# Performance work log

Measured on AMD Instinct MI355X. Metric: run time of the kernel, lower is better.

## Reference

```python
import jax, jax.numpy as jnp
import numpy as np

B, S, D, H = 2, 2048, 1024, 16
HD = D // H  # head_dim = 64


def setup_inputs() -> dict:
    key = jax.random.key(0)
    ks = jax.random.split(key, 6)
    scale = 0.02
    x = jax.random.normal(ks[0], (B, S, D), dtype=jnp.float32)
    Wq = jax.random.normal(ks[1], (D, D), dtype=jnp.float32) * scale
    Wk = jax.random.normal(ks[2], (D, D), dtype=jnp.float32) * scale
    Wv = jax.random.normal(ks[3], (D, D), dtype=jnp.float32) * scale
    Wo = jax.random.normal(ks[4], (D, D), dtype=jnp.float32) * scale
    bo = jnp.zeros((D,), dtype=jnp.float32)
    return {"x": x, "Wq": Wq, "Wk": Wk, "Wv": Wv, "Wo": Wo, "bo": bo}


def reference(x, Wq, Wk, Wv, Wo, bo):
    b, s, _ = x.shape
    # Linear projections (qkv_bias=False), split into heads: [b, h, s, hd]
    def split_heads(t):
        return t.reshape(b, s, H, HD).transpose(0, 2, 1, 3)
    q = split_heads(x @ Wq)
    k = split_heads(x @ Wk)
    v = split_heads(x @ Wv)
    # Scaled dot-product scores: [b, h, s, s]
    scores = jnp.einsum('bhqd,bhkd->bhqk', q, k) / jnp.sqrt(jnp.float32(HD))
    # Causal mask: triu(ones, diagonal=1) positions -> -inf
    causal = jnp.triu(jnp.ones((s, s), dtype=bool), k=1)
    scores = jnp.where(causal, -jnp.inf, scores)
    attn = jax.nn.softmax(scores, axis=-1)
    # dropout p=0.0 (eval-equivalent): identity
    ctx = jnp.einsum('bhqk,bhkd->bhqd', attn, v)  # [b, h, s, hd]
    ctx = ctx.transpose(0, 2, 1, 3).reshape(b, s, D)
    return ctx @ Wo + bo
```

## Files before the change

kernel.cpp:

```cpp
#include <hip/hip_runtime.h>
#include <math.h>

#define BB 2
#define SS 2048
#define DD 1024
#define HH 16
#define HD 64
#define MM (BB * SS)

typedef __bf16 bf16;
typedef __attribute__((ext_vector_type(8))) __bf16 bf16x8;
typedef __attribute__((ext_vector_type(4))) __bf16 bf16x4;
typedef __attribute__((ext_vector_type(4))) short short4v;
typedef __attribute__((ext_vector_type(4))) float f32x4;

#if __has_builtin(__builtin_amdgcn_exp2f)
#define EXP2F(x) __builtin_amdgcn_exp2f(x)
#else
#define EXP2F(x) exp2f(x)
#endif

__device__ __forceinline__ f32x4 pv_mfma16(bf16x4 a, short4v b, f32x4 c) {
    return __builtin_amdgcn_mfma_f32_16x16x16bf16_1k(
        __builtin_bit_cast(short4v, a), b, c, 0, 0, 0);
}

__device__ __forceinline__ void gld_lds16(const void* g, void* l) {
    __builtin_amdgcn_global_load_lds(
        (const __attribute__((address_space(1))) void*)g,
        (__attribute__((address_space(3))) void*)l, 16, 0, 0);
}

__global__ __launch_bounds__(256) void prep(
    const float* __restrict__ x,
    const float* __restrict__ W0, const float* __restrict__ W1,
    const float* __restrict__ W2, const float* __restrict__ W3,
    bf16* __restrict__ xb, bf16* __restrict__ Wt)
{
    __shared__ float tile[32][33];
    const int z = blockIdx.z;
    if (z < 4) {
        const float* W = (z == 0) ? W0 : (z == 1) ? W1 : (z == 2) ? W2 : W3;
        bf16* O = Wt + (size_t)z * DD * DD;
        const int tx = threadIdx.x & 31, ty = threadIdx.x >> 5;
        const int k0 = blockIdx.y * 32, n0 = blockIdx.x * 32;
#pragma unroll
        for (int i = 0; i < 4; ++i)
            tile[ty + i * 8][tx] = W[(size_t)(k0 + ty + i * 8) * DD + n0 + tx];
        __syncthreads();
#pragma unroll
        for (int i = 0; i < 4; ++i)
            O[(size_t)(n0 + ty + i * 8) * DD + k0 + tx] = (bf16)tile[tx][ty + i * 8];
    } else {
        const int lb = (z - 4) * 1024 + blockIdx.y * 32 + blockIdx.x;
        const size_t i = ((size_t)lb * 256 + threadIdx.x) * 8;
        const float4 a = *(const float4*)(x + i);
        const float4 b = *(const float4*)(x + i + 4);
        bf16x8 o;
        o[0] = (bf16)a.x; o[1] = (bf16)a.y; o[2] = (bf16)a.z; o[3] = (bf16)a.w;
        o[4] = (bf16)b.x; o[5] = (bf16)b.y; o[6] = (bf16)b.z; o[7] = (bf16)b.w;
        *(bf16x8*)(xb + i) = o;
    }
}

__device__ __forceinline__ void mfma_core(
    const bf16* __restrict__ A, const bf16* __restrict__ Bt,
    int bm, int bn, int K, bf16* As, bf16* Bs, f32x4 (&acc)[4][4])
{
    const int t = threadIdx.x;
    const int w = t >> 6;
    const int l16 = t & 15, quad = (t >> 4) & 3;
    const int wr = w >> 1, wc = w & 1;
    const int arow = t >> 2;
    const int achk = (((t & 3) ^ ((t >> 3) & 3)) << 3);

    const bf16* gA = A + (size_t)(bm + arow) * K + achk;
    const bf16* gB = Bt + (size_t)(bn + arow) * K + achk;
    bf16* lA = As + w * 512;
    bf16* lB = Bs + w * 512;

    const int swz = (l16 >> 1) & 3;
    int offA[4], offB[4];
#pragma unroll
    for (int i = 0; i < 4; ++i) {
        offA[i] = (wr * 64 + i * 16 + l16) * 32 + ((quad ^ swz) << 3);
        offB[i] = (wc * 64 + i * 16 + l16) * 32 + ((quad ^ swz) << 3);
    }

#define GSTAGE(BUF, KO) do {                                                  \
        gld_lds16(gA + (KO),                  lA + (BUF) * 4096);             \
        gld_lds16(gA + (size_t)64 * K + (KO), lA + (BUF) * 4096 + 2048);      \
        gld_lds16(gB + (KO),                  lB + (BUF) * 4096);             \
        gld_lds16(gB + (size_t)64 * K + (KO), lB + (BUF) * 4096 + 2048);      \
    } while (0)

#define GCOMPUTE(BUF) do {                                                    \
        const bf16* Ab = As + (BUF) * 4096;                                   \
        const bf16* Bb = Bs + (BUF) * 4096;                                   \
        bf16x8 af[4], bv[4];                                                  \
        _Pragma("unroll")                                                     \
        for (int i = 0; i < 4; ++i) {                                         \
            af[i] = *(const bf16x8*)(Ab + offA[i]);                           \
            bv[i] = *(const bf16x8*)(Bb + offB[i]);                           \
        }                                                                     \
        _Pragma("unroll")                                                     \
        for (int mi = 0; mi < 4; ++mi)                                        \
            _Pragma("unroll")                                                 \
            for (int ni = 0; ni < 4; ++ni)                                    \
                acc[mi][ni] = __builtin_amdgcn_mfma_f32_16x16x32_bf16(        \
                    af[mi], bv[ni], acc[mi][ni], 0, 0, 0);                    \
    } while (0)

#define GBAR() do {                                                           \
        asm volatile("s_barrier" ::: "memory");                               \
        __builtin_amdgcn_sched_barrier(0);                                    \
    } while (0)

    GSTAGE(0, 0);
    const int nk = K >> 5;
    for (int kt = 0; kt < nk; kt += 2) {
        GSTAGE(1, (kt + 1) << 5);
        asm volatile("s_waitcnt vmcnt(4)" ::: "memory");
        GBAR();
        GCOMPUTE(0);
        asm volatile("s_waitcnt lgkmcnt(0)" ::: "memory");
        GBAR();
        if (kt + 2 < nk) {
            GSTAGE(0, (kt + 2) << 5);
            asm volatile("s_waitcnt vmcnt(4)" ::: "memory");
        } else {
            asm volatile("s_waitcnt vmcnt(0)" ::: "memory");
        }
        GBAR();
        GCOMPUTE(1);
        asm volatile("s_waitcnt lgkmcnt(0)" ::: "memory");
        GBAR();
    }
#undef GBAR
#undef GCOMPUTE
#undef GSTAGE
}

__global__ __launch_bounds__(256) void gemm_qkv(
    const bf16* __restrict__ xb, const bf16* __restrict__ Wt,
    bf16* __restrict__ Qb, bf16* __restrict__ Kb, bf16* __restrict__ Vb)
{
    __shared__ __align__(16) bf16 As[2 * 128 * 32];
    __shared__ __align__(16) bf16 Bs[2 * 128 * 32];
    const int bm = blockIdx.y * 128, bn = blockIdx.x * 128, z = blockIdx.z;

    f32x4 acc[4][4] = {};
    mfma_core(xb, Wt + (size_t)z * DD * DD, bm, bn, DD, As, Bs, acc);

    const int t = threadIdx.x;
    const int w = t >> 6, l16 = t & 15, quad = (t >> 4) & 3;
    const int wr = w >> 1, wc = w & 1;
    bf16* outp = (z == 0) ? Qb : (z == 1) ? Kb : Vb;
    const float scl = (z == 0) ? 0.18033688011f : 1.0f;

#pragma unroll
    for (int mi = 0; mi < 4; ++mi) {
#pragma unroll
        for (int ni = 0; ni < 4; ++ni) {
            const int col = bn + wc * 64 + ni * 16 + l16;
            const int h = col >> 6, hd = col & 63;
#pragma unroll
            for (int r = 0; r < 4; ++r) {
                const int row = bm + wr * 64 + mi * 16 + quad * 4 + r;
                const int b = row >> 11, s = row & (SS - 1);
                size_t addr;
                if (z < 2) addr = ((size_t)((b * HH + h) * SS + s)) * HD + hd;
                else       addr = ((size_t)((b * HH + h) * HD + hd)) * SS + s;
                outp[addr] = (bf16)(acc[mi][ni][r] * scl);
            }
        }
    }
}

__global__ __launch_bounds__(256) void gemm_out(
    const bf16* __restrict__ ctx, const bf16* __restrict__ Wto,
    const float* __restrict__ bias, float* __restrict__ out)
{
    __shared__ __align__(16) bf16 As[2 * 128 * 32];
    __shared__ __align__(16) bf16 Bs[2 * 128 * 32];
    const int bm = blockIdx.y * 128, bn = blockIdx.x * 128;

    f32x4 acc[4][4] = {};
    mfma_core(ctx, Wto, bm, bn, DD, As, Bs, acc);

    const int t = threadIdx.x;
    const int w = t >> 6, l16 = t & 15, quad = (t >> 4) & 3;
    const int wr = w >> 1, wc = w & 1;

#pragma unroll
    for (int mi = 0; mi < 4; ++mi) {
#pragma unroll
        for (int ni = 0; ni < 4; ++ni) {
            const int col = bn + wc * 64 + ni * 16 + l16;
            const float b = bias[col];
#pragma unroll
            for (int r = 0; r < 4; ++r) {
                const int row = bm + wr * 64 + mi * 16 + quad * 4 + r;
                out[(size_t)row * DD + col] = acc[mi][ni][r] + b;
            }
        }
    }
}

__global__ __launch_bounds__(256, 4) void attn_flash(
    const bf16* __restrict__ Q, const bf16* __restrict__ K,
    const bf16* __restrict__ Vt, bf16* __restrict__ ctx)
{
    __shared__ __align__(16) bf16 Ks[2][64 * 64];
    __shared__ __align__(16) bf16 Vs[2][64 * 64];

    const int t = threadIdx.x;
    const int w = t >> 6;
    const int lane = t & 63;
    const int l16 = lane & 15, quad = lane >> 4;

    const int L  = blockIdx.x;
    const int bh = L & 31;
    const int idx = L >> 5;
    const int pg = idx >> 3, pr = idx & 7;
    const int qg = (pg == 0) ? 31 - pr : (pg == 1) ? pr
                 : (pg == 2) ? 23 - pr : 8 + pr;
    const int q0b = qg * 64;
    const int q0w = q0b + w * 16;
    const int qrow = q0w + l16;
    const int nkt = qg + 1;

    const bf16* Qp = Q  + ((size_t)bh * SS + q0w) * HD;
    const bf16* Kp = K  + (size_t)bh * SS * HD;
    const bf16* Vp = Vt + (size_t)bh * HD * SS;

    const bf16x8 bQ0 = *(const bf16x8*)(Qp + l16 * HD + quad * 8);
    const bf16x8 bQ1 = *(const bf16x8*)(Qp + l16 * HD + 32 + quad * 8);

    const int r8 = lane >> 3, cs = lane & 7;
    const int rowA = (w * 2) * 8 + r8, rowB = (w * 2 + 1) * 8 + r8;
    const int cA = (cs - rowA) & 7, cB = (cs - rowB) & 7;
    const bf16* gK0 = Kp + (size_t)rowA * HD + cA * 8;
    const bf16* gK1 = Kp + (size_t)rowB * HD + cB * 8;
    const bf16* gV0 = Vp + (size_t)rowA * SS + cA * 8;
    const bf16* gV1 = Vp + (size_t)rowB * SS + cB * 8;
    bf16* const lK0 = &Ks[0][(w * 2) * 512];
    bf16* const lK1 = &Ks[0][(w * 2 + 1) * 512];
    bf16* const lV0 = &Vs[0][(w * 2) * 512];
    bf16* const lV1 = &Vs[0][(w * 2 + 1) * 512];

#define STAGE(BUF, KB) do {                                              \
        gld_lds16(gK0 + (size_t)(KB) * HD, lK0 + (BUF) * 4096);          \
        gld_lds16(gK1 + (size_t)(KB) * HD, lK1 + (BUF) * 4096);          \
        gld_lds16(gV0 + (KB),              lV0 + (BUF) * 4096);          \
        gld_lds16(gV1 + (KB),              lV1 + (BUF) * 4096);          \
    } while (0)

    const int offK0 = l16 * 64 + ((quad + l16) & 7) * 8;
    const int offK1 = l16 * 64 + ((quad + 4 + l16) & 7) * 8;
    int offV[4];
#pragma unroll
    for (int mi = 0; mi < 4; ++mi)
        offV[mi] = l16 * 64 + ((((quad >> 1) + 2 * mi + l16) & 7) * 8)
                 + (quad & 1) * 4;

    const bf16* const KsB = &Ks[0][0];
    const bf16* const VsB = &Vs[0][0];

    f32x4 accO[4] = {{0,0,0,0},{0,0,0,0},{0,0,0,0},{0,0,0,0}};
    float Lr = 0.f;

#define TILE(BUF, KB) do {                                                   \
        f32x4 St[4] = {{0,0,0,0},{0,0,0,0},{0,0,0,0},{0,0,0,0}};             \
        _Pragma("unroll")                                                    \
        for (int mi = 0; mi < 4; ++mi) {                                     \
            const bf16x8 a0 = *(const bf16x8*)(KsB + (BUF) * 4096            \
                                               + mi * 1024 + offK0);         \
            const bf16x8 a1 = *(const bf16x8*)(KsB + (BUF) * 4096            \
                                               + mi * 1024 + offK1);         \
            St[mi] = __builtin_amdgcn_mfma_f32_16x16x32_bf16(                \
                a0, bQ0, St[mi], 0, 0, 0);                                   \
            St[mi] = __builtin_amdgcn_mfma_f32_16x16x32_bf16(                \
                a1, bQ1, St[mi], 0, 0, 0);                                   \
        }                                                                    \
        if ((KB) + 63 > q0w) {                                               \
            _Pragma("unroll")                                                \
            for (int mi = 0; mi < 4; ++mi)                                   \
                _Pragma("unroll")                                            \
                for (int rr = 0; rr < 4; ++rr)                               \
                    if ((KB) + mi * 16 + quad * 4 + rr > qrow)               \
                        St[mi][rr] = -1e30f;                                 \
        }                                                                    \
        float rs = 0.f;                                                      \
        short4v pb[4];                                                       \
        _Pragma("unroll")                                                    \
        for (int mi = 0; mi < 4; ++mi) {                                     \
            bf16x4 pk;                                                       \
            _Pragma("unroll")                                                \
            for (int rr = 0; rr < 4; ++rr) {                                 \
                const float p = EXP2F(St[mi][rr]);                           \
                rs += p;                                                     \
                pk[rr] = (bf16)p;                                            \
            }                                                                \
            pb[mi] = __builtin_bit_cast(short4v, pk);                        \
        }                                                                    \
        rs += __shfl_xor(rs, 16);                                            \
        rs += __shfl_xor(rs, 32);                                            \
        Lr += rs;                                                            \
        _Pragma("unroll")                                                    \
        for (int mi = 0; mi < 4; ++mi) {                                     \
            _Pragma("unroll")                                                \
            for (int db = 0; db < 4; ++db) {                                 \
                const bf16x4 aV = *(const bf16x4*)(VsB + (BUF) * 4096        \
                                                   + db * 1024 + offV[mi]);  \
                accO[db] = pv_mfma16(aV, pb[mi], accO[db]);                  \
            }                                                                \
        }                                                                    \
    } while (0)

    STAGE(0, 0);
    int kb = 0;
    for (int kt = 0; kt + 2 <= nkt; kt += 2) {
        __syncthreads();
        STAGE(1, kb + 64);
        TILE(0, kb);
        __syncthreads();
        if (kt + 2 < nkt) STAGE(0, kb + 128);
        TILE(1, kb + 64);
        kb += 128;
    }
    if (nkt & 1) {
        __syncthreads();
        TILE(0, kb);
    }
#undef TILE
#undef STAGE

    const float rinv = 1.0f / Lr;
    const int b = bh >> 4, h = bh & (HH - 1);
    bf16* op = ctx + ((size_t)(b * SS + q0w + l16)) * DD + h * HD;
#pragma unroll
    for (int db = 0; db < 4; ++db) {
        bf16x4 o;
#pragma unroll
        for (int rr = 0; rr < 4; ++rr) o[rr] = (bf16)(accO[db][rr] * rinv);
        *(bf16x4*)(op + db * 16 + quad * 4) = o;
    }
}

extern "C" void kernel_launch(void* const* d_in, const int* in_sizes, int n_in,
                              void* d_out, int out_size, void* d_ws, size_t ws_size,
                              hipStream_t stream)
{
    const float* x  = (const float*)d_in[0];
    const float* Wq = (const float*)d_in[1];
    const float* Wk = (const float*)d_in[2];
    const float* Wv = (const float*)d_in[3];
    const float* Wo = (const float*)d_in[4];
    const float* bo = (const float*)d_in[5];
    float* out = (float*)d_out;

    const size_t chunk = (size_t)MM * DD;
    bf16* xb  = (bf16*)d_ws;
    bf16* Wt  = xb + chunk;
    bf16* Qb  = Wt + 4 * (size_t)DD * DD;
    bf16* Kb  = Qb + chunk;
    bf16* Vb  = Kb + chunk;
    bf16* ctx = Vb + chunk;

    prep<<<dim3(32, 32, 6), dim3(256), 0, stream>>>(x, Wq, Wk, Wv, Wo, xb, Wt);

    gemm_qkv<<<dim3(DD / 128, MM / 128, 3), dim3(256), 0, stream>>>(xb, Wt, Qb, Kb, Vb);

    attn_flash<<<dim3(BB * HH * (SS / 64)), dim3(256), 0, stream>>>(Qb, Kb, Vb, ctx);

    gemm_out<<<dim3(DD / 128, MM / 128), dim3(256), 0, stream>>>(
        ctx, Wt + 3 * (size_t)DD * DD, bo, out);
}
```

Baseline: 182.9 us.

## Rewrite QKV GEMM with 256x256 tiles, 8 waves and interleaved pipelined staging

Replaces the shared 128x128 GEMM core for the QKV projection with a dedicated 256x256-tile kernel using 512 threads (8 waves, each owning 128x64). It uses 16x16x32 MFMA, swizzled LDS layout, double-buffered async global-to-LDS loads interleaved between MFMA half-steps, and raises wave priority around the MFMA blocks. The aim is more data reuse per load and better overlap of memory with compute. The trade-off is higher register and LDS use, and a grid of only 192 blocks, which may underfill the CUs.

```diff
diff --git a/kernel.cpp b/kernel.cpp
--- a/kernel.cpp
+++ b/kernel.cpp
@@ -141,32 +141,129 @@
 #undef GSTAGE
 }
 
-__global__ __launch_bounds__(256) void gemm_qkv(
+__global__ __launch_bounds__(512, 2) void gemm_qkv(
     const bf16* __restrict__ xb, const bf16* __restrict__ Wt,
     bf16* __restrict__ Qb, bf16* __restrict__ Kb, bf16* __restrict__ Vb)
 {
-    __shared__ __align__(16) bf16 As[2 * 128 * 32];
-    __shared__ __align__(16) bf16 Bs[2 * 128 * 32];
-    const int bm = blockIdx.y * 128, bn = blockIdx.x * 128, z = blockIdx.z;
-
-    f32x4 acc[4][4] = {};
-    mfma_core(xb, Wt + (size_t)z * DD * DD, bm, bn, DD, As, Bs, acc);
+    __shared__ __align__(16) bf16 As[2 * 16384];
+    __shared__ __align__(16) bf16 Bs[2 * 16384];
 
     const int t = threadIdx.x;
-    const int w = t >> 6, l16 = t & 15, quad = (t >> 4) & 3;
-    const int wr = w >> 1, wc = w & 1;
+    const int w = t >> 6, lane = t & 63;
+    const int l16 = lane & 15, quad = (lane >> 4) & 3;
+    const int wr = w >> 2, wc = w & 3;
+    const int bm = blockIdx.y * 256, bn = blockIdx.x * 256, z = blockIdx.z;
+
+    const bf16* Ag = xb;
+    const bf16* Bg = Wt + (size_t)z * DD * DD;
+
+    const int srow = t >> 2;
+    const int gsw = ((t & 3) ^ ((t >> 3) & 3)) << 3;
+    const bf16* gA0 = Ag + (size_t)(bm + srow) * DD + gsw;
+    const bf16* gA1 = Ag + (size_t)(bm + 128 + srow) * DD + gsw;
+    const bf16* gB0 = Bg + (size_t)(bn + srow) * DD + gsw;
+    const bf16* gB1 = Bg + (size_t)(bn + 128 + srow) * DD + gsw;
+    bf16* const sA = As + t * 8;
+    bf16* const sB = Bs + t * 8;
+
+    const int swz = (l16 >> 1) & 3;
+    const int rbA = (wr * 128 + l16) * 32 + ((quad ^ swz) << 3);
+    const int rbB = (wc * 64 + l16) * 32 + ((quad ^ swz) << 3);
+
+    f32x4 acc[8][4] = {};
+    bf16x8 afr[4], bfr[4];
+
+#define QSTAGE(GP0, GP1, SP, BUF, KH, TOFF) do {                              \
+        gld_lds16((GP0) + (TOFF) + (KH) * 32,                                 \
+                  (SP) + (BUF) * 16384 + (KH) * 8192);                        \
+        gld_lds16((GP1) + (TOFF) + (KH) * 32,                                 \
+                  (SP) + (BUF) * 16384 + (KH) * 8192 + 4096);                 \
+    } while (0)
+
+#define QREAD_A(BUF, MIH, KK) do {                                           \
+        _Pragma("unroll")                                                    \
+        for (int j = 0; j < 4; ++j)                                          \
+            afr[j] = *(const bf16x8*)(As + (BUF) * 16384 + (KK) * 8192       \
+                                      + rbA + (MIH) * 2048 + j * 512);       \
+    } while (0)
+
+#define QREAD_B(BUF, KK) do {                                                \
+        _Pragma("unroll")                                                    \
+        for (int ni = 0; ni < 4; ++ni)                                       \
+            bfr[ni] = *(const bf16x8*)(Bs + (BUF) * 16384 + (KK) * 8192      \
+                                       + rbB + ni * 512);                    \
+    } while (0)
+
+#define QMFMA(MIH) do {                                                      \
+        __builtin_amdgcn_s_setprio(1);                                       \
+        _Pragma("unroll")                                                    \
+        for (int j = 0; j < 4; ++j)                                          \
+            _Pragma("unroll")                                                 \
+            for (int ni = 0; ni < 4; ++ni)                                   \
+                acc[(MIH) * 4 + j][ni] =                                     \
+                    __builtin_amdgcn_mfma_f32_16x16x32_bf16(                 \
+                        afr[j], bfr[ni], acc[(MIH) * 4 + j][ni], 0, 0, 0);   \
+        __builtin_amdgcn_s_setprio(0);                                       \
+    } while (0)
+
+#define QTILE(BUF, TNEXT, STG) do {                                          \
+                                                         \
+        asm volatile("s_waitcnt vmcnt(4)" ::: "memory");                     \
+        asm volatile("s_barrier" ::: "memory");                              \
+        __builtin_amdgcn_sched_barrier(0);                                   \
+        if (STG) QSTAGE(gA0, gA1, sA, (BUF) ^ 1, 0, TNEXT);                  \
+        QREAD_B(BUF, 0);                                                     \
+        QREAD_A(BUF, 0, 0);                                                  \
+        QMFMA(0);                                                            \
+                                                         \
+        if (STG) QSTAGE(gB0, gB1, sB, (BUF) ^ 1, 0, TNEXT);                  \
+        QREAD_A(BUF, 1, 0);                                                  \
+        QMFMA(1);                                                            \
+                                                         \
+        if (STG) {                                                           \
+            QSTAGE(gA0, gA1, sA, (BUF) ^ 1, 1, TNEXT);                       \
+            asm volatile("s_waitcnt vmcnt(6)" ::: "memory");                 \
+        } else {                                                             \
+            asm volatile("s_waitcnt vmcnt(0)" ::: "memory");                 \
+        }                                                                    \
+        asm volatile("s_barrier" ::: "memory");                              \
+        __builtin_amdgcn_sched_barrier(0);                                   \
+        QREAD_B(BUF, 1);                                                     \
+        QREAD_A(BUF, 0, 1);                                                  \
+        QMFMA(0);                                                            \
+                                                         \
+        if (STG) QSTAGE(gB0, gB1, sB, (BUF) ^ 1, 1, TNEXT);                  \
+        QREAD_A(BUF, 1, 1);                                                  \
+        QMFMA(1);                                                            \
+    } while (0)
+
+    QSTAGE(gA0, gA1, sA, 0, 0, 0);
+    QSTAGE(gB0, gB1, sB, 0, 0, 0);
+    QSTAGE(gA0, gA1, sA, 0, 1, 0);
+    QSTAGE(gB0, gB1, sB, 0, 1, 0);
+
+    for (int T = 0; T < 16; T += 2) {
+        QTILE(0, (T + 1) * 64, 1);
+        QTILE(1, (T + 2) * 64, (T + 2) < 16);
+    }
+#undef QTILE
+#undef QMFMA
+#undef QREAD_B
+#undef QREAD_A
+#undef QSTAGE
+
     bf16* outp = (z == 0) ? Qb : (z == 1) ? Kb : Vb;
     const float scl = (z == 0) ? 0.18033688011f : 1.0f;
 
 #pragma unroll
-    for (int mi = 0; mi < 4; ++mi) {
+    for (int mi = 0; mi < 8; ++mi) {
 #pragma unroll
         for (int ni = 0; ni < 4; ++ni) {
             const int col = bn + wc * 64 + ni * 16 + l16;
             const int h = col >> 6, hd = col & 63;
 #pragma unroll
             for (int r = 0; r < 4; ++r) {
-                const int row = bm + wr * 64 + mi * 16 + quad * 4 + r;
+                const int row = bm + wr * 128 + mi * 16 + quad * 4 + r;
                 const int b = row >> 11, s = row & (SS - 1);
                 size_t addr;
                 if (z < 2) addr = ((size_t)((b * HH + h) * SS + s)) * HD + hd;
@@ -309,7 +406,7 @@
         Lr += rs;                                                            \
         _Pragma("unroll")                                                    \
         for (int mi = 0; mi < 4; ++mi) {                                     \
-            _Pragma("unroll")                                                \
+            _Pragma("unroll")                                                 \
             for (int db = 0; db < 4; ++db) {                                 \
                 const bf16x4 aV = *(const bf16x4*)(VsB + (BUF) * 4096        \
                                                    + db * 1024 + offV[mi]);  \
@@ -370,7 +467,7 @@
 
     prep<<<dim3(32, 32, 6), dim3(256), 0, stream>>>(x, Wq, Wk, Wv, Wo, xb, Wt);
 
-    gemm_qkv<<<dim3(DD / 128, MM / 128, 3), dim3(256), 0, stream>>>(xb, Wt, Qb, Kb, Vb);
+    gemm_qkv<<<dim3(DD / 256, MM / 256, 3), dim3(512), 0, stream>>>(xb, Wt, Qb, Kb, Vb);
 
     attn_flash<<<dim3(BB * HH * (SS / 64)), dim3(256), 0, stream>>>(Qb, Kb, Vb, ctx);
 
```

After: 198.9 us. 1.09x slower.

## Rewrite QKV GEMM with 256x256 tiles, 8 waves, and split-phase LDS pipeline

Applied to the files above, without the earlier changes.

Replaces the shared 128x128 mfma_core path for the QKV projection with a dedicated 256x256 tile kernel using 512 threads (8 waves, each computing 128x64). It stages 64-wide K slices into double-buffered, XOR-swizzled LDS, and interleaves LDS reads, global prefetch and 16x16x32 MFMAs in four sub-phases per K tile, raising wave priority around the MFMAs. The goal is more data reuse per LDS byte and better overlap of memory with math. In exchange it uses far more LDS and registers, and the grid shrinks to 192 blocks, which may leave compute units idle.

```diff
diff --git a/kernel.cpp b/kernel.cpp
--- a/kernel.cpp
+++ b/kernel.cpp
@@ -141,32 +141,140 @@
 #undef GSTAGE
 }
 
-__global__ __launch_bounds__(256) void gemm_qkv(
+__global__ __launch_bounds__(512, 2) void gemm_qkv(
     const bf16* __restrict__ xb, const bf16* __restrict__ Wt,
     bf16* __restrict__ Qb, bf16* __restrict__ Kb, bf16* __restrict__ Vb)
 {
-    __shared__ __align__(16) bf16 As[2 * 128 * 32];
-    __shared__ __align__(16) bf16 Bs[2 * 128 * 32];
-    const int bm = blockIdx.y * 128, bn = blockIdx.x * 128, z = blockIdx.z;
-
-    f32x4 acc[4][4] = {};
-    mfma_core(xb, Wt + (size_t)z * DD * DD, bm, bn, DD, As, Bs, acc);
+    __shared__ __align__(16) bf16 As[2][2][128 * 64];
+    __shared__ __align__(16) bf16 Bs[2][2][128 * 64];
 
     const int t = threadIdx.x;
-    const int w = t >> 6, l16 = t & 15, quad = (t >> 4) & 3;
-    const int wr = w >> 1, wc = w & 1;
+    const int w = t >> 6, lane = t & 63;
+    const int l16 = lane & 15, quad = (lane >> 4) & 3;
+    const int wr = w >> 2, wc = w & 3;
+    const int bm = blockIdx.y * 256, bn = blockIdx.x * 256, z = blockIdx.z;
+
+    const bf16* Ag = xb;
+    const bf16* Bg = Wt + (size_t)z * DD * DD;
+    bf16* const aLds = &As[0][0][0];
+    bf16* const bLds = &Bs[0][0][0];
+
+    const int sr = t >> 3;
+    const int sg = ((t & 7) ^ (sr & 7)) << 3;
+
+#define STG_A(BUF, H, TT) do {                                                \
+        gld_lds16(Ag + (size_t)(bm + (H) * 128 + sr) * DD + (TT) * 64 + sg,   \
+                  aLds + (BUF) * 16384 + (H) * 8192 + t * 8);                 \
+        gld_lds16(Ag + (size_t)(bm + (H) * 128 + 64 + sr) * DD + (TT) * 64 + sg, \
+                  aLds + (BUF) * 16384 + (H) * 8192 + 4096 + t * 8);          \
+    } while (0)
+#define STG_B(BUF, H, TT) do {                                                \
+        gld_lds16(Bg + (size_t)(bn + (H) * 128 + sr) * DD + (TT) * 64 + sg,   \
+                  bLds + (BUF) * 16384 + (H) * 8192 + t * 8);                 \
+        gld_lds16(Bg + (size_t)(bn + (H) * 128 + 64 + sr) * DD + (TT) * 64 + sg, \
+                  bLds + (BUF) * 16384 + (H) * 8192 + 4096 + t * 8);          \
+    } while (0)
+
+    const int csw = l16 & 7;
+    const int ck0 = (quad ^ csw) << 3;
+    const int ck1 = ((quad + 4) ^ csw) << 3;
+    const int abase = wr * 8192 + l16 * 64;
+    const int bbase = (wc >> 1) * 8192 + ((wc & 1) * 64 + l16) * 64;
+
+    f32x4 acc[8][4] = {};
+    bf16x8 aF[8][2];
+    bf16x8 bF[2][2];
+
+#define RD_A(BUF, MIH) do {                                                   \
+        _Pragma("unroll")                                                     \
+        for (int j = 0; j < 4; ++j) {                                         \
+            aF[(MIH) * 4 + j][0] = *(const bf16x8*)(aLds + (BUF) * 16384      \
+                + abase + ((MIH) * 4 + j) * 1024 + ck0);                      \
+            aF[(MIH) * 4 + j][1] = *(const bf16x8*)(aLds + (BUF) * 16384      \
+                + abase + ((MIH) * 4 + j) * 1024 + ck1);                      \
+        }                                                                     \
+    } while (0)
+#define RD_B(BUF, NIH) do {                                                   \
+        _Pragma("unroll")                                                     \
+        for (int n = 0; n < 2; ++n) {                                         \
+            bF[n][0] = *(const bf16x8*)(bLds + (BUF) * 16384 + bbase          \
+                + ((NIH) * 2 + n) * 1024 + ck0);                              \
+            bF[n][1] = *(const bf16x8*)(bLds + (BUF) * 16384 + bbase          \
+                + ((NIH) * 2 + n) * 1024 + ck1);                              \
+        }                                                                     \
+    } while (0)
+#define MM16(MIH, NIH) do {                                                   \
+        __builtin_amdgcn_s_setprio(1);                                        \
+        _Pragma("unroll")                                                     \
+        for (int j = 0; j < 4; ++j)                                           \
+            _Pragma("unroll")                                                 \
+            for (int n = 0; n < 2; ++n)                                       \
+                _Pragma("unroll")                                             \
+                for (int k = 0; k < 2; ++k)                                   \
+                    acc[(MIH) * 4 + j][(NIH) * 2 + n] =                       \
+                        __builtin_amdgcn_mfma_f32_16x16x32_bf16(              \
+                            aF[(MIH) * 4 + j][k], bF[n][k],                   \
+                            acc[(MIH) * 4 + j][(NIH) * 2 + n], 0, 0, 0);      \
+        __builtin_amdgcn_s_setprio(0);                                        \
+    } while (0)
+#define QBAR() do { asm volatile("s_barrier" ::: "memory");                   \
+                    __builtin_amdgcn_sched_barrier(0); } while (0)
+#define QLG0() do { asm volatile("s_waitcnt lgkmcnt(0)" ::: "memory");        \
+                    __builtin_amdgcn_sched_barrier(0); } while (0)
+
+#define QTILE(U, TT, SB, SA, VMC) do {                                        \
+                                  \
+        RD_A(U, 0); RD_B(U, 0);                                               \
+        if (SB) STG_B((U) ^ 1, 0, (TT) + 1);                                  \
+        QBAR(); QLG0(); MM16(0, 0); QBAR();                                   \
+                                              \
+        RD_A(U, 1);                                                           \
+        if (SB) STG_B((U) ^ 1, 1, (TT) + 1);                                  \
+        QBAR(); QLG0(); MM16(1, 0); QBAR();                                   \
+                  \
+        RD_B(U, 1);                                                           \
+        if (SA) STG_A(U, 0, (TT) + 2);                                        \
+        QBAR(); QLG0(); MM16(0, 1); QBAR();                                   \
+                \
+        if (SA) STG_A(U, 1, (TT) + 2);                                        \
+        if (VMC) asm volatile("s_waitcnt vmcnt(4)" ::: "memory");             \
+        else     asm volatile("s_waitcnt vmcnt(0)" ::: "memory");             \
+        QBAR(); MM16(1, 1); QBAR();                                           \
+    } while (0)
+
+    STG_A(0, 0, 0); STG_A(0, 1, 0);
+    STG_B(0, 0, 0); STG_B(0, 1, 0);
+    STG_A(1, 0, 1); STG_A(1, 1, 1);
+    asm volatile("s_waitcnt vmcnt(4)" ::: "memory");
+    QBAR();
+
+    for (int T = 0; T < 14; T += 2) {
+        QTILE(0, T, 1, 1, 1);
+        QTILE(1, T + 1, 1, 1, 1);
+    }
+    QTILE(0, 14, 1, 0, 0);
+    QTILE(1, 15, 0, 0, 0);
+#undef QTILE
+#undef QLG0
+#undef QBAR
+#undef MM16
+#undef RD_B
+#undef RD_A
+#undef STG_B
+#undef STG_A
+
     bf16* outp = (z == 0) ? Qb : (z == 1) ? Kb : Vb;
     const float scl = (z == 0) ? 0.18033688011f : 1.0f;
 
 #pragma unroll
-    for (int mi = 0; mi < 4; ++mi) {
+    for (int mi = 0; mi < 8; ++mi) {
 #pragma unroll
         for (int ni = 0; ni < 4; ++ni) {
             const int col = bn + wc * 64 + ni * 16 + l16;
             const int h = col >> 6, hd = col & 63;
 #pragma unroll
             for (int r = 0; r < 4; ++r) {
-                const int row = bm + wr * 64 + mi * 16 + quad * 4 + r;
+                const int row = bm + wr * 128 + mi * 16 + quad * 4 + r;
                 const int b = row >> 11, s = row & (SS - 1);
                 size_t addr;
                 if (z < 2) addr = ((size_t)((b * HH + h) * SS + s)) * HD + hd;
@@ -309,7 +417,7 @@
         Lr += rs;                                                            \
         _Pragma("unroll")                                                    \
         for (int mi = 0; mi < 4; ++mi) {                                     \
-            _Pragma("unroll")                                                \
+            _Pragma("unroll")                                                 \
             for (int db = 0; db < 4; ++db) {                                 \
                 const bf16x4 aV = *(const bf16x4*)(VsB + (BUF) * 4096        \
                                                    + db * 1024 + offV[mi]);  \
@@ -370,7 +478,7 @@
 
     prep<<<dim3(32, 32, 6), dim3(256), 0, stream>>>(x, Wq, Wk, Wv, Wo, xb, Wt);
 
-    gemm_qkv<<<dim3(DD / 128, MM / 128, 3), dim3(256), 0, stream>>>(xb, Wt, Qb, Kb, Vb);
+    gemm_qkv<<<dim3(DD / 256, MM / 256, 3), dim3(512), 0, stream>>>(xb, Wt, Qb, Kb, Vb);
 
     attn_flash<<<dim3(BB * HH * (SS / 64)), dim3(256), 0, stream>>>(Qb, Kb, Vb, ctx);
 
```

Measured after the change: 205.7 us. 1.12x slower.
